# Performance work log

Hardware: AMD Instinct MI355X
Metric: run time of the kernel (lower is better)

## Reference

```python
import jax, jax.numpy as jnp
import numpy as np

TEMPERATURE = 0.07


def setup_inputs() -> dict:
    key = jax.random.key(0)
    k1, k2 = jax.random.split(key)
    B, V, C, H, W = 4, 2, 128, 32, 32
    features = jax.random.normal(k1, (B, V, C, H, W), dtype=jnp.float32)
    # L2-normalize per-pixel feature vectors (channel dim), as contrastive
    # embeddings are in practice; the original exp() is unstabilized.
    features = features / jnp.linalg.norm(features, axis=2, keepdims=True)
    labels = jax.random.randint(k2, (B, V, H, W), 0, 4, dtype=jnp.int32)
    return {"features": features, "labels": labels}


def reference(features, labels):
    B, V, C, H, W = features.shape
    # torch.cat(torch.unbind(features, dim=1), dim=0): views stacked along batch
    cf = jnp.transpose(features, (1, 0, 2, 3, 4)).reshape(B * V, C, H, W)
    # kernels = cf.permute(0,2,3,1).reshape(-1, C, 1, 1); conv2d with 1x1 kernels
    # == pairwise dot products of per-pixel feature vectors.
    X = jnp.transpose(cf, (0, 2, 3, 1)).reshape(-1, C)  # [N, C], N = B*V*H*W
    N = X.shape[0]
    logits = (X @ X.T) / TEMPERATURE  # [N, N]

    lab = jnp.transpose(labels, (1, 0, 2, 3)).reshape(-1)  # [N]
    mask = (lab[:, None] == lab[None, :]).astype(logits.dtype)  # [N, N]
    logits_mask = 1.0 - jnp.eye(N, dtype=logits.dtype)  # zero the diagonal
    mask = mask * logits_mask

    exp_logits = jnp.exp(logits) * logits_mask
    log_prob = logits - jnp.log(jnp.sum(exp_logits, axis=1, keepdims=True))
    mean_log_prob_pos = jnp.sum(mask * log_prob, axis=1) / jnp.sum(mask, axis=1)
    loss = -mean_log_prob_pos  # [N]

    non_bg = (lab != 0).astype(logits.dtype)
    return jnp.sum(loss * non_bg) / jnp.sum(non_bg)
```

## Files before the change

### kernel.cpp

```cpp
#include <hip/hip_runtime.h>
#include <hip/hip_bf16.h>
#include <stdint.h>

typedef short bf16x8 __attribute__((ext_vector_type(8)));
typedef float f32x16 __attribute__((ext_vector_type(16)));

#define NROWS 8192
#define CDIM  128
#define TEMP  0.07f
#define C1F   20.6099291555566248f

#define OFF_S    0
#define OFF_G    32768
#define OFF_HIST (32768 + 2048)
#define OFF_SUM  (32768 + 2048 + 16)
#define OFF_TKT  (32768 + 2048 + 16 + 4)
#define ZBYTES   (32768 + 2048 + 16 + 4 + 4)
#define ZWORDS   (ZBYTES / 4)
#define OFF_GPART (ZBYTES + 8)
#define OFF_CPART (OFF_GPART + 256 * 512 * 4)

__device__ __forceinline__ float bf2f(unsigned short u) {
  union { unsigned int i; float f; } x; x.i = ((unsigned int)u) << 16; return x.f;
}
__device__ __forceinline__ unsigned short f2bf(float f) {
  union { float f; unsigned int i; } x; x.f = f;
  unsigned int r = x.i + 0x7fffu + ((x.i >> 16) & 1u);
  return (unsigned short)(r >> 16);
}
__device__ __forceinline__ float fexp2(float x) {
#if __has_builtin(__builtin_amdgcn_exp2f)
  return __builtin_amdgcn_exp2f(x);
#else
  return exp2f(x);
#endif
}

__global__ __launch_bounds__(256) void k_pack(const float* __restrict__ F,
                                              const int* __restrict__ labels,
                                              unsigned short* __restrict__ Xb,
                                              float* __restrict__ zbase,
                                              float* __restrict__ Gpart,
                                              int* __restrict__ Cpart) {
  const int tid = threadIdx.x;
  {
    int idx = blockIdx.x * 256 + tid;
    if (idx < ZWORDS) zbase[idx] = 0.0f;
  }
  __shared__ float lds[128 * 33];
  __shared__ int   slab[32];
  __shared__ float gred[4][128];
  const int g   = blockIdx.x >> 5;
  const int hw0 = (blockIdx.x & 31) << 5;
  if (tid < 32) slab[tid] = labels[g * 1024 + hw0 + tid];
#pragma unroll
  for (int p = 0; p < 16; ++p) {
    int c  = p * 8 + (tid >> 5);
    int hw = hw0 + (tid & 31);
    lds[c * 33 + (tid & 31)] = F[(g * 128 + c) * 1024 + hw];
  }
  __syncthreads();
#pragma unroll
  for (int p = 0; p < 16; ++p) {
    int hwl = p * 2 + (tid >> 7);
    int c   = tid & 127;
    int row = g * 1024 + hw0 + hwl;
    Xb[row * 128 + c] = f2bf(lds[c * 33 + hwl]);
  }
  const int c  = tid & 127;
  const int rh = tid >> 7;
  float a0 = 0.f, a1 = 0.f, a2 = 0.f, a3 = 0.f;
#pragma unroll
  for (int k = 0; k < 16; ++k) {
    int   hwl = rh * 16 + k;
    float v   = lds[c * 33 + hwl];
    int   lab = slab[hwl];
    a0 += (lab == 0) ? v : 0.f;
    a1 += (lab == 1) ? v : 0.f;
    a2 += (lab == 2) ? v : 0.f;
    a3 += (lab == 3) ? v : 0.f;
  }
  if (rh == 1) { gred[0][c] = a0; gred[1][c] = a1; gred[2][c] = a2; gred[3][c] = a3; }
  if (tid >= 32 && tid < 36) {
    int j = tid - 32, cnt = 0;
#pragma unroll
    for (int k2 = 0; k2 < 32; ++k2) cnt += (slab[k2] == j);
    Cpart[blockIdx.x * 4 + j] = cnt;
  }
  __syncthreads();
  if (rh == 0) {
    float* gp = Gpart + blockIdx.x * 512;
    gp[0 * 128 + c] = a0 + gred[0][c];
    gp[1 * 128 + c] = a1 + gred[1][c];
    gp[2 * 128 + c] = a2 + gred[2][c];
    gp[3 * 128 + c] = a3 + gred[3][c];
  }
}

__global__ __launch_bounds__(256, 2) void k_main(const unsigned short* __restrict__ Xb,
                                                 float* __restrict__ S,
                                                 float* __restrict__ G,
                                                 int* __restrict__ hist,
                                                 const float* __restrict__ Gpart,
                                                 const int* __restrict__ Cpart) {
  __shared__ int4 ldsB[2][2][16 * 33];
  const int bid  = blockIdx.x;
  const int tid  = threadIdx.x;
  const int lane = tid & 63;

  if (bid >= 512) {
    const int rb = bid - 512;
    const int l  = tid & 63;
    const int w  = tid >> 6;
    const float* gp = Gpart + (w * 64) * 512 + rb * 64 + l;
    float s = 0.f;
#pragma unroll 8
    for (int k = 0; k < 64; ++k) s += gp[k * 512];
    __shared__ float red[4][64];
    red[w][l] = s;
    __syncthreads();
    if (w == 0) G[rb * 64 + l] = red[0][l] + red[1][l] + red[2][l] + red[3][l];
    if (rb == 0) {
      int4 c4 = ((const int4*)Cpart)[tid];
      for (int mm = 1; mm < 64; mm <<= 1) {
        c4.x += __shfl_xor(c4.x, mm, 64);
        c4.y += __shfl_xor(c4.y, mm, 64);
        c4.z += __shfl_xor(c4.z, mm, 64);
        c4.w += __shfl_xor(c4.w, mm, 64);
      }
      __shared__ int hred[4][4];
      if (l == 0) { hred[w][0] = c4.x; hred[w][1] = c4.y; hred[w][2] = c4.z; hred[w][3] = c4.w; }
      __syncthreads();
      if (tid < 4) hist[tid] = hred[0][tid] + hred[1][tid] + hred[2][tid] + hred[3][tid];
    }
    return;
  }

  const int wave = tid >> 6;
  const int m    = lane & 31;
  const int half = lane >> 5;

  int  rowA, rowB, colBase, NT;
  bool isPair;
  if (bid < 496) {
    isPair = false;
    const int k = bid;
    int a = (int)((63.0f - sqrtf(3969.0f - 8.0f * (float)k)) * 0.5f);
    while ((63 * (a + 1) - (a + 1) * (a + 1)) / 2 <= k) ++a;
    while ((63 * a - a * a) / 2 > k) --a;
    const int b = a + 1 + (k - (63 * a - a * a) / 2);
    rowA    = a * 256 + wave * 32;
    rowB    = a * 256 + (7 - wave) * 32;
    colBase = b * 256;
    NT      = 4;
  } else {
    isPair = true;
    const int d = bid - 496;
    rowA    = d * 512 + wave * 32;
    rowB    = d * 512 + (7 - wave) * 32;
    colBase = d * 512;
    NT      = 8;
  }

  bf16x8 afrag0[8], afrag1[8];
#pragma unroll
  for (int s = 0; s < 8; ++s) {
    afrag0[s] = *(const bf16x8*)(Xb + (rowA + m) * CDIM + (half + 2 * s) * 8);
    afrag1[s] = *(const bf16x8*)(Xb + (rowB + m) * CDIM + (half + 2 * s) * 8);
  }

  float accS0[16], accS1[16];
#pragma unroll
  for (int r = 0; r < 16; ++r) { accS0[r] = 0.f; accS1[r] = 0.f; }

  auto flushRows = [&](int rA, int rB) {
#pragma unroll
    for (int r = 0; r < 16; ++r) {
      float v = accS0[r];
      v += __shfl_xor(v, 1, 64);  v += __shfl_xor(v, 2, 64);
      v += __shfl_xor(v, 4, 64);  v += __shfl_xor(v, 8, 64);
      v += __shfl_xor(v, 16, 64);
      float v2 = accS1[r];
      v2 += __shfl_xor(v2, 1, 64); v2 += __shfl_xor(v2, 2, 64);
      v2 += __shfl_xor(v2, 4, 64); v2 += __shfl_xor(v2, 8, 64);
      v2 += __shfl_xor(v2, 16, 64);
      if (m == 0) {
        int rowoff = (r & 3) + 8 * (r >> 2) + 4 * half;
        atomicAdd(&S[rA + rowoff], v);
        atomicAdd(&S[rB + rowoff], v2);
      }
      accS0[r] = 0.f; accS1[r] = 0.f;
    }
  };

  const int n_l = tid >> 3;
  const int bq  = tid & 7;
  const unsigned short* src = Xb + (colBase + n_l) * CDIM + bq * 16;
  int4 v0 = *(const int4*)src;
  int4 v1 = *(const int4*)(src + 8);
  int4 v2 = *(const int4*)(src + 32 * CDIM);
  int4 v3 = *(const int4*)(src + 32 * CDIM + 8);
  ldsB[0][0][(2 * bq) * 33 + n_l]     = v0;
  ldsB[0][0][(2 * bq + 1) * 33 + n_l] = v1;
  ldsB[0][1][(2 * bq) * 33 + n_l]     = v2;
  ldsB[0][1][(2 * bq + 1) * 33 + n_l] = v3;
  src += 64 * CDIM;
  v0 = *(const int4*)src;
  v1 = *(const int4*)(src + 8);
  v2 = *(const int4*)(src + 32 * CDIM);
  v3 = *(const int4*)(src + 32 * CDIM + 8);

  for (int t = 0; t < NT; ++t) {
    __syncthreads();
    if (isPair && t == 4) {
      flushRows(rowA, rowB);
      rowA += 256; rowB += 256;
#pragma unroll
      for (int s = 0; s < 8; ++s) {
        afrag0[s] = *(const bf16x8*)(Xb + (rowA + m) * CDIM + (half + 2 * s) * 8);
        afrag1[s] = *(const bf16x8*)(Xb + (rowB + m) * CDIM + (half + 2 * s) * 8);
      }
    }
    if (t < NT - 1) {
      const int nb = (t + 1) & 1;
      ldsB[nb][0][(2 * bq) * 33 + n_l]     = v0;
      ldsB[nb][0][(2 * bq + 1) * 33 + n_l] = v1;
      ldsB[nb][1][(2 * bq) * 33 + n_l]     = v2;
      ldsB[nb][1][(2 * bq + 1) * 33 + n_l] = v3;
    }
    if (t < NT - 2) {
      src += 64 * CDIM;
      v0 = *(const int4*)src;
      v1 = *(const int4*)(src + 8);
      v2 = *(const int4*)(src + 32 * CDIM);
      v3 = *(const int4*)(src + 32 * CDIM + 8);
    }
    const int cur = t & 1;
#pragma unroll
    for (int u = 0; u < 2; ++u) {
      const int cb = (2 * t + u) & 7;
      bool doA, doB, maskA, maskB;
      if (isPair) {
        doA = (cb >= wave);         maskA = (cb == wave);
        doB = (cb >= 7 - wave);     maskB = (cb == 7 - wave);
      } else {
        doA = true; doB = true; maskA = false; maskB = false;
      }
      float csum = 0.f;
      if (doA) {
        f32x16 acc;
#pragma unroll
        for (int r = 0; r < 16; ++r) acc[r] = 0.f;
#pragma unroll
        for (int s = 0; s < 8; ++s) {
          bf16x8 bfrag = *(const bf16x8*)&ldsB[cur][u][(half + 2 * s) * 33 + m];
          acc = __builtin_amdgcn_mfma_f32_32x32x16_bf16(afrag0[s], bfrag, acc, 0, 0, 0);
        }
        if (maskA) {
#pragma unroll
          for (int r = 0; r < 16; ++r) {
            int rowoff = (r & 3) + 8 * (r >> 2) + 4 * half;
            float e = (rowoff == m) ? 0.f : fexp2(acc[r] * C1F);
            accS0[r] += e;
          }
        } else {
#pragma unroll
          for (int r = 0; r < 16; ++r) {
            float e = fexp2(acc[r] * C1F);
            accS0[r] += e;
            csum += e;
          }
        }
      }
      if (doB) {
        f32x16 acc;
#pragma unroll
        for (int r = 0; r < 16; ++r) acc[r] = 0.f;
#pragma unroll
        for (int s = 0; s < 8; ++s) {
          bf16x8 bfrag = *(const bf16x8*)&ldsB[cur][u][(half + 2 * s) * 33 + m];
          acc = __builtin_amdgcn_mfma_f32_32x32x16_bf16(afrag1[s], bfrag, acc, 0, 0, 0);
        }
        if (maskB) {
#pragma unroll
          for (int r = 0; r < 16; ++r) {
            int rowoff = (r & 3) + 8 * (r >> 2) + 4 * half;
            float e = (rowoff == m) ? 0.f : fexp2(acc[r] * C1F);
            accS1[r] += e;
          }
        } else {
#pragma unroll
          for (int r = 0; r < 16; ++r) {
            float e = fexp2(acc[r] * C1F);
            accS1[r] += e;
            csum += e;
          }
        }
      }
      if ((doA && !maskA) || (doB && !maskB)) {
        float v = csum + __shfl_xor(csum, 32, 64);
        if (half == 0) atomicAdd(&S[colBase + (2 * t + u) * 32 + m], v);
      }
    }
  }

  flushRows(rowA, rowB);
}

__global__ __launch_bounds__(256) void k_loss(const unsigned short* __restrict__ Xb,
                                              const int* __restrict__ labels,
                                              const float* __restrict__ S,
                                              const float* __restrict__ G,
                                              const int* __restrict__ hist,
                                              float* __restrict__ sumLoss,
                                              int* __restrict__ ticket,
                                              float* __restrict__ out) {
  const int i   = blockIdx.x * 256 + threadIdx.x;
  const int lab = labels[i];
  const float* g = G + lab * 128;
  const unsigned short* x = Xb + i * CDIM;
  float dot = 0.f, nrm = 0.f;
#pragma unroll
  for (int cc = 0; cc < 16; ++cc) {
    int4 q = *(const int4*)(x + cc * 8);
    const unsigned int* qs = (const unsigned int*)&q;
#pragma unroll
    for (int j = 0; j < 4; ++j) {
      unsigned int u = qs[j];
      float lo = __uint_as_float(u << 16);
      float hi = __uint_as_float(u & 0xffff0000u);
      int   ci = cc * 8 + j * 2;
      dot += lo * g[ci] + hi * g[ci + 1];
      nrm += lo * lo + hi * hi;
    }
  }
  float Si   = S[i];
  float cnt  = (float)(hist[lab] - 1);
  float loss = logf(Si) - (dot - nrm) / (TEMP * cnt);
  float contrib = (lab != 0) ? loss : 0.f;
  for (int mm = 1; mm < 64; mm <<= 1) contrib += __shfl_xor(contrib, mm, 64);
  __shared__ float ws4[4];
  if ((threadIdx.x & 63) == 0) ws4[threadIdx.x >> 6] = contrib;
  __syncthreads();
  if (threadIdx.x == 0) {
    atomicAdd(sumLoss, ws4[0] + ws4[1] + ws4[2] + ws4[3]);
    __threadfence();
    int t = atomicAdd(ticket, 1);
    if (t == 31) {
      float total = atomicAdd(sumLoss, 0.0f);
      out[0] = total / (float)(NROWS - hist[0]);
    }
  }
}

extern "C" void kernel_launch(void* const* d_in, const int* in_sizes, int n_in,
                              void* d_out, int out_size, void* d_ws, size_t ws_size,
                              hipStream_t stream) {
  const float* F      = (const float*)d_in[0];
  const int*   labels = (const int*)d_in[1];
  char* ws = (char*)d_ws;

  unsigned short* Xb      = (unsigned short*)ws;
  const size_t    offS    = (size_t)NROWS * CDIM * 2;
  float*          S       = (float*)(ws + offS + OFF_S);
  float*          G       = (float*)(ws + offS + OFF_G);
  int*            hist    = (int*)(ws + offS + OFF_HIST);
  float*          sumLoss = (float*)(ws + offS + OFF_SUM);
  int*            ticket  = (int*)(ws + offS + OFF_TKT);
  float*          Gpart   = (float*)(ws + offS + OFF_GPART);
  int*            Cpart   = (int*)(ws + offS + OFF_CPART);

  hipLaunchKernelGGL(k_pack, dim3(256), dim3(256), 0, stream, F, labels, Xb, S, Gpart, Cpart);
  hipLaunchKernelGGL(k_main, dim3(520), dim3(256), 0, stream, Xb, S, G, hist, Gpart, Cpart);
  hipLaunchKernelGGL(k_loss, dim3(32), dim3(256), 0, stream, Xb, labels, S, G, hist,
                     sumLoss, ticket, (float*)d_out);
}
```

Measured before the change: 96.95 us.

## Split off-diagonal and diagonal tile paths, interleave MFMAs, accumulate column sums in registers

The off-diagonal blocks now get their own fully unrolled path. Each wave owns 64 contiguous rows and issues two MFMA chains per B fragment, interleaved. Column exp-sums are kept in registers and flushed with atomics once at the end instead of per sub-tile, and the tile index search becomes a simple loop. The diagonal blocks also preload B fragments once for both row halves and defer the column atomics to the phase flush. This is meant to cut per-subtile atomics, LDS reloads and branch overhead, at the cost of more registers.

```diff
diff --git a/kernel.cpp b/kernel.cpp
--- a/kernel.cpp
+++ b/kernel.cpp
@@ -139,41 +139,87 @@
   const int wave = tid >> 6;
   const int m    = lane & 31;
   const int half = lane >> 5;
-
-  int  rowA, rowB, colBase, NT;
-  bool isPair;
+  const int n_l  = tid >> 3;
+  const int bq   = tid & 7;
+
   if (bid < 496) {
-    isPair = false;
-    const int k = bid;
-    int a = (int)((63.0f - sqrtf(3969.0f - 8.0f * (float)k)) * 0.5f);
-    while ((63 * (a + 1) - (a + 1) * (a + 1)) / 2 <= k) ++a;
-    while ((63 * a - a * a) / 2 > k) --a;
-    const int b = a + 1 + (k - (63 * a - a * a) / 2);
-    rowA    = a * 256 + wave * 32;
-    rowB    = a * 256 + (7 - wave) * 32;
-    colBase = b * 256;
-    NT      = 4;
-  } else {
-    isPair = true;
-    const int d = bid - 496;
-    rowA    = d * 512 + wave * 32;
-    rowB    = d * 512 + (7 - wave) * 32;
-    colBase = d * 512;
-    NT      = 8;
-  }
-
-  bf16x8 afrag0[8], afrag1[8];
-#pragma unroll
-  for (int s = 0; s < 8; ++s) {
-    afrag0[s] = *(const bf16x8*)(Xb + (rowA + m) * CDIM + (half + 2 * s) * 8);
-    afrag1[s] = *(const bf16x8*)(Xb + (rowB + m) * CDIM + (half + 2 * s) * 8);
-  }
-
-  float accS0[16], accS1[16];
-#pragma unroll
-  for (int r = 0; r < 16; ++r) { accS0[r] = 0.f; accS1[r] = 0.f; }
-
-  auto flushRows = [&](int rA, int rB) {
+    int a = 0, cum = 0;
+    while (cum + (31 - a) <= bid) { cum += 31 - a; ++a; }
+    const int b       = a + 1 + (bid - cum);
+    const int r0      = a * 256 + wave * 64;
+    const int colBase = b * 256;
+
+    bf16x8 afrag0[8], afrag1[8];
+#pragma unroll
+    for (int s = 0; s < 8; ++s) {
+      afrag0[s] = *(const bf16x8*)(Xb + (r0 + m) * CDIM + (half + 2 * s) * 8);
+      afrag1[s] = *(const bf16x8*)(Xb + (r0 + 32 + m) * CDIM + (half + 2 * s) * 8);
+    }
+
+    float accS0[16], accS1[16], colAcc[8];
+#pragma unroll
+    for (int r = 0; r < 16; ++r) { accS0[r] = 0.f; accS1[r] = 0.f; }
+#pragma unroll
+    for (int k = 0; k < 8; ++k) colAcc[k] = 0.f;
+
+    const unsigned short* src = Xb + (colBase + n_l) * CDIM + bq * 16;
+    int4 v0 = *(const int4*)src;
+    int4 v1 = *(const int4*)(src + 8);
+    int4 v2 = *(const int4*)(src + 32 * CDIM);
+    int4 v3 = *(const int4*)(src + 32 * CDIM + 8);
+    ldsB[0][0][(2 * bq) * 33 + n_l]     = v0;
+    ldsB[0][0][(2 * bq + 1) * 33 + n_l] = v1;
+    ldsB[0][1][(2 * bq) * 33 + n_l]     = v2;
+    ldsB[0][1][(2 * bq + 1) * 33 + n_l] = v3;
+    src += 64 * CDIM;
+    v0 = *(const int4*)src;
+    v1 = *(const int4*)(src + 8);
+    v2 = *(const int4*)(src + 32 * CDIM);
+    v3 = *(const int4*)(src + 32 * CDIM + 8);
+
+#pragma unroll
+    for (int t = 0; t < 4; ++t) {
+      __syncthreads();
+      if (t < 3) {
+        const int nb = (t + 1) & 1;
+        ldsB[nb][0][(2 * bq) * 33 + n_l]     = v0;
+        ldsB[nb][0][(2 * bq + 1) * 33 + n_l] = v1;
+        ldsB[nb][1][(2 * bq) * 33 + n_l]     = v2;
+        ldsB[nb][1][(2 * bq + 1) * 33 + n_l] = v3;
+      }
+      if (t < 2) {
+        src += 64 * CDIM;
+        v0 = *(const int4*)src;
+        v1 = *(const int4*)(src + 8);
+        v2 = *(const int4*)(src + 32 * CDIM);
+        v3 = *(const int4*)(src + 32 * CDIM + 8);
+      }
+      const int cur = t & 1;
+#pragma unroll
+      for (int u = 0; u < 2; ++u) {
+        f32x16 acc0, acc1;
+#pragma unroll
+        for (int r = 0; r < 16; ++r) { acc0[r] = 0.f; acc1[r] = 0.f; }
+#pragma unroll
+        for (int s = 0; s < 8; ++s) {
+          bf16x8 bfrag = *(const bf16x8*)&ldsB[cur][u][(half + 2 * s) * 33 + m];
+          acc0 = __builtin_amdgcn_mfma_f32_32x32x16_bf16(afrag0[s], bfrag, acc0, 0, 0, 0);
+          acc1 = __builtin_amdgcn_mfma_f32_32x32x16_bf16(afrag1[s], bfrag, acc1, 0, 0, 0);
+        }
+        float cs0 = 0.f, cs1 = 0.f;
+#pragma unroll
+        for (int r = 0; r < 16; ++r) {
+          float e0 = fexp2(acc0[r] * C1F);
+          float e1 = fexp2(acc1[r] * C1F);
+          accS0[r] += e0;
+          accS1[r] += e1;
+          cs0 += e0;
+          cs1 += e1;
+        }
+        colAcc[2 * t + u] = cs0 + cs1;
+      }
+    }
+
 #pragma unroll
     for (int r = 0; r < 16; ++r) {
       float v = accS0[r];
@@ -186,125 +232,168 @@
       v2 += __shfl_xor(v2, 16, 64);
       if (m == 0) {
         int rowoff = (r & 3) + 8 * (r >> 2) + 4 * half;
-        atomicAdd(&S[rA + rowoff], v);
-        atomicAdd(&S[rB + rowoff], v2);
-      }
-      accS0[r] = 0.f; accS1[r] = 0.f;
-    }
-  };
-
-  const int n_l = tid >> 3;
-  const int bq  = tid & 7;
-  const unsigned short* src = Xb + (colBase + n_l) * CDIM + bq * 16;
-  int4 v0 = *(const int4*)src;
-  int4 v1 = *(const int4*)(src + 8);
-  int4 v2 = *(const int4*)(src + 32 * CDIM);
-  int4 v3 = *(const int4*)(src + 32 * CDIM + 8);
-  ldsB[0][0][(2 * bq) * 33 + n_l]     = v0;
-  ldsB[0][0][(2 * bq + 1) * 33 + n_l] = v1;
-  ldsB[0][1][(2 * bq) * 33 + n_l]     = v2;
-  ldsB[0][1][(2 * bq + 1) * 33 + n_l] = v3;
-  src += 64 * CDIM;
-  v0 = *(const int4*)src;
-  v1 = *(const int4*)(src + 8);
-  v2 = *(const int4*)(src + 32 * CDIM);
-  v3 = *(const int4*)(src + 32 * CDIM + 8);
-
-  for (int t = 0; t < NT; ++t) {
-    __syncthreads();
-    if (isPair && t == 4) {
-      flushRows(rowA, rowB);
-      rowA += 256; rowB += 256;
-#pragma unroll
-      for (int s = 0; s < 8; ++s) {
-        afrag0[s] = *(const bf16x8*)(Xb + (rowA + m) * CDIM + (half + 2 * s) * 8);
-        afrag1[s] = *(const bf16x8*)(Xb + (rowB + m) * CDIM + (half + 2 * s) * 8);
-      }
-    }
-    if (t < NT - 1) {
-      const int nb = (t + 1) & 1;
-      ldsB[nb][0][(2 * bq) * 33 + n_l]     = v0;
-      ldsB[nb][0][(2 * bq + 1) * 33 + n_l] = v1;
-      ldsB[nb][1][(2 * bq) * 33 + n_l]     = v2;
-      ldsB[nb][1][(2 * bq + 1) * 33 + n_l] = v3;
-    }
-    if (t < NT - 2) {
-      src += 64 * CDIM;
-      v0 = *(const int4*)src;
-      v1 = *(const int4*)(src + 8);
-      v2 = *(const int4*)(src + 32 * CDIM);
-      v3 = *(const int4*)(src + 32 * CDIM + 8);
-    }
-    const int cur = t & 1;
-#pragma unroll
-    for (int u = 0; u < 2; ++u) {
-      const int cb = (2 * t + u) & 7;
-      bool doA, doB, maskA, maskB;
-      if (isPair) {
-        doA = (cb >= wave);         maskA = (cb == wave);
-        doB = (cb >= 7 - wave);     maskB = (cb == 7 - wave);
-      } else {
-        doA = true; doB = true; maskA = false; maskB = false;
-      }
-      float csum = 0.f;
-      if (doA) {
-        f32x16 acc;
-#pragma unroll
-        for (int r = 0; r < 16; ++r) acc[r] = 0.f;
+        atomicAdd(&S[r0 + rowoff], v);
+        atomicAdd(&S[r0 + 32 + rowoff], v2);
+      }
+    }
+#pragma unroll
+    for (int k = 0; k < 8; ++k) {
+      float v = colAcc[k] + __shfl_xor(colAcc[k], 32, 64);
+      if (half == 0) atomicAdd(&S[colBase + k * 32 + m], v);
+    }
+    return;
+  }
+
+  {
+    const int d = bid - 496;
+    int rowA    = d * 512 + wave * 32;
+    int rowB    = d * 512 + (7 - wave) * 32;
+    int colBase = d * 512;
+
+    bf16x8 afrag0[8], afrag1[8];
+#pragma unroll
+    for (int s = 0; s < 8; ++s) {
+      afrag0[s] = *(const bf16x8*)(Xb + (rowA + m) * CDIM + (half + 2 * s) * 8);
+      afrag1[s] = *(const bf16x8*)(Xb + (rowB + m) * CDIM + (half + 2 * s) * 8);
+    }
+
+    float accS0[16], accS1[16], colAcc[8];
+#pragma unroll
+    for (int r = 0; r < 16; ++r) { accS0[r] = 0.f; accS1[r] = 0.f; }
+#pragma unroll
+    for (int k = 0; k < 8; ++k) colAcc[k] = 0.f;
+
+    auto flushPhase = [&](int rA, int rB, int cB) {
+#pragma unroll
+      for (int r = 0; r < 16; ++r) {
+        float v = accS0[r];
+        v += __shfl_xor(v, 1, 64);  v += __shfl_xor(v, 2, 64);
+        v += __shfl_xor(v, 4, 64);  v += __shfl_xor(v, 8, 64);
+        v += __shfl_xor(v, 16, 64);
+        float v2 = accS1[r];
+        v2 += __shfl_xor(v2, 1, 64); v2 += __shfl_xor(v2, 2, 64);
+        v2 += __shfl_xor(v2, 4, 64); v2 += __shfl_xor(v2, 8, 64);
+        v2 += __shfl_xor(v2, 16, 64);
+        if (m == 0) {
+          int rowoff = (r & 3) + 8 * (r >> 2) + 4 * half;
+          atomicAdd(&S[rA + rowoff], v);
+          atomicAdd(&S[rB + rowoff], v2);
+        }
+        accS0[r] = 0.f; accS1[r] = 0.f;
+      }
+#pragma unroll
+      for (int k = 0; k < 8; ++k) {
+        float v = colAcc[k] + __shfl_xor(colAcc[k], 32, 64);
+        if (half == 0) atomicAdd(&S[cB + k * 32 + m], v);
+        colAcc[k] = 0.f;
+      }
+    };
+
+    const unsigned short* src = Xb + (colBase + n_l) * CDIM + bq * 16;
+    int4 v0 = *(const int4*)src;
+    int4 v1 = *(const int4*)(src + 8);
+    int4 v2 = *(const int4*)(src + 32 * CDIM);
+    int4 v3 = *(const int4*)(src + 32 * CDIM + 8);
+    ldsB[0][0][(2 * bq) * 33 + n_l]     = v0;
+    ldsB[0][0][(2 * bq + 1) * 33 + n_l] = v1;
+    ldsB[0][1][(2 * bq) * 33 + n_l]     = v2;
+    ldsB[0][1][(2 * bq + 1) * 33 + n_l] = v3;
+    src += 64 * CDIM;
+    v0 = *(const int4*)src;
+    v1 = *(const int4*)(src + 8);
+    v2 = *(const int4*)(src + 32 * CDIM);
+    v3 = *(const int4*)(src + 32 * CDIM + 8);
+
+#pragma unroll
+    for (int t = 0; t < 8; ++t) {
+      __syncthreads();
+      if (t == 4) {
+        flushPhase(rowA, rowB, colBase);
+        rowA += 256; rowB += 256; colBase += 256;
 #pragma unroll
         for (int s = 0; s < 8; ++s) {
-          bf16x8 bfrag = *(const bf16x8*)&ldsB[cur][u][(half + 2 * s) * 33 + m];
-          acc = __builtin_amdgcn_mfma_f32_32x32x16_bf16(afrag0[s], bfrag, acc, 0, 0, 0);
+          afrag0[s] = *(const bf16x8*)(Xb + (rowA + m) * CDIM + (half + 2 * s) * 8);
+          afrag1[s] = *(const bf16x8*)(Xb + (rowB + m) * CDIM + (half + 2 * s) * 8);
         }
-        if (maskA) {
-#pragma unroll
-          for (int r = 0; r < 16; ++r) {
-            int rowoff = (r & 3) + 8 * (r >> 2) + 4 * half;
-            float e = (rowoff == m) ? 0.f : fexp2(acc[r] * C1F);
-            accS0[r] += e;
+      }
+      if (t < 7) {
+        const int nb = (t + 1) & 1;
+        ldsB[nb][0][(2 * bq) * 33 + n_l]     = v0;
+        ldsB[nb][0][(2 * bq + 1) * 33 + n_l] = v1;
+        ldsB[nb][1][(2 * bq) * 33 + n_l]     = v2;
+        ldsB[nb][1][(2 * bq + 1) * 33 + n_l] = v3;
+      }
+      if (t < 6) {
+        src += 64 * CDIM;
+        v0 = *(const int4*)src;
+        v1 = *(const int4*)(src + 8);
+        v2 = *(const int4*)(src + 32 * CDIM);
+        v3 = *(const int4*)(src + 32 * CDIM + 8);
+      }
+      const int cur = t & 1;
+#pragma unroll
+      for (int u = 0; u < 2; ++u) {
+        const int cb = (2 * t + u) & 7;
+        const bool actA = (cb >= wave);
+        const bool actB = (cb >= 7 - wave);
+        if (actA || actB) {
+          bf16x8 bf[8];
+#pragma unroll
+          for (int s = 0; s < 8; ++s)
+            bf[s] = *(const bf16x8*)&ldsB[cur][u][(half + 2 * s) * 33 + m];
+          float cs = 0.f;
+          if (actA) {
+            f32x16 acc;
+#pragma unroll
+            for (int r = 0; r < 16; ++r) acc[r] = 0.f;
+#pragma unroll
+            for (int s = 0; s < 8; ++s)
+              acc = __builtin_amdgcn_mfma_f32_32x32x16_bf16(afrag0[s], bf[s], acc, 0, 0, 0);
+            if (cb == wave) {
+#pragma unroll
+              for (int r = 0; r < 16; ++r) {
+                int rowoff = (r & 3) + 8 * (r >> 2) + 4 * half;
+                float e = (rowoff == m) ? 0.f : fexp2(acc[r] * C1F);
+                accS0[r] += e;
+              }
+            } else {
+#pragma unroll
+              for (int r = 0; r < 16; ++r) {
+                float e = fexp2(acc[r] * C1F);
+                accS0[r] += e;
+                cs += e;
+              }
+            }
           }
-        } else {
-#pragma unroll
-          for (int r = 0; r < 16; ++r) {
-            float e = fexp2(acc[r] * C1F);
-            accS0[r] += e;
-            csum += e;
+          if (actB) {
+            f32x16 acc;
+#pragma unroll
+            for (int r = 0; r < 16; ++r) acc[r] = 0.f;
+#pragma unroll
+            for (int s = 0; s < 8; ++s)
+              acc = __builtin_amdgcn_mfma_f32_32x32x16_bf16(afrag1[s], bf[s], acc, 0, 0, 0);
+            if (cb == 7 - wave) {
+#pragma unroll
+              for (int r = 0; r < 16; ++r) {
+                int rowoff = (r & 3) + 8 * (r >> 2) + 4 * half;
+                float e = (rowoff == m) ? 0.f : fexp2(acc[r] * C1F);
+                accS1[r] += e;
+              }
+            } else {
+#pragma unroll
+              for (int r = 0; r < 16; ++r) {
+                float e = fexp2(acc[r] * C1F);
+                accS1[r] += e;
+                cs += e;
+              }
+            }
           }
+          colAcc[cb] += cs;
         }
       }
-      if (doB) {
-        f32x16 acc;
-#pragma unroll
-        for (int r = 0; r < 16; ++r) acc[r] = 0.f;
-#pragma unroll
-        for (int s = 0; s < 8; ++s) {
-          bf16x8 bfrag = *(const bf16x8*)&ldsB[cur][u][(half + 2 * s) * 33 + m];
-          acc = __builtin_amdgcn_mfma_f32_32x32x16_bf16(afrag1[s], bfrag, acc, 0, 0, 0);
-        }
-        if (maskB) {
-#pragma unroll
-          for (int r = 0; r < 16; ++r) {
-            int rowoff = (r & 3) + 8 * (r >> 2) + 4 * half;
-            float e = (rowoff == m) ? 0.f : fexp2(acc[r] * C1F);
-            accS1[r] += e;
-          }
-        } else {
-#pragma unroll
-          for (int r = 0; r < 16; ++r) {
-            float e = fexp2(acc[r] * C1F);
-            accS1[r] += e;
-            csum += e;
-          }
-        }
-      }
-      if ((doA && !maskA) || (doB && !maskB)) {
-        float v = csum + __shfl_xor(csum, 32, 64);
-        if (half == 0) atomicAdd(&S[colBase + (2 * t + u) * 32 + m], v);
-      }
-    }
-  }
-
-  flushRows(rowA, rowB);
+    }
+    flushPhase(rowA, rowB, colBase);
+  }
 }
 
 __global__ __launch_bounds__(256) void k_loss(const unsigned short* __restrict__ Xb,
```

Result: slower. 153.0 us (+57.8%).
